# Optimization experiments

Measured on AMD Instinct MI355X. Metric: run time of the kernel, lower is better.

Reference implementation:

```python
import jax, jax.numpy as jnp
import numpy as np

B, S, K, N, GROUP = 4, 8, 4096, 11008, 128
NUM_GROUPS = K // GROUP  # 32


def setup_inputs() -> dict:
    key = jax.random.key(0)
    k1, k2, k3 = jax.random.split(key, 3)
    x = jax.random.normal(k1, (B, S, K), dtype=jnp.float16)
    # packed int4 weights: each byte holds two nibbles (low nibble = even k, high = odd k)
    weight_packed = jax.random.randint(k2, (N, K // 2), 0, 256, dtype=jnp.int32)
    # scales: abs(randn)*0.1 in fp16, as in the torch module
    scales = (jnp.abs(jax.random.normal(k3, (N, NUM_GROUPS), dtype=jnp.float16)) * jnp.float16(0.1))
    return {"x": x, "weight_packed": weight_packed, "scales": scales}


def _dequant(weight_packed, scales, Kd):
    # unpack: low nibble -> even index k, high nibble -> odd index k+1
    n = weight_packed.shape[0]
    low = weight_packed & 0xF
    high = (weight_packed >> 4) & 0xF
    w = jnp.stack([low, high], axis=-1).reshape(n, Kd)  # [N, K] int in [0,16)
    g = Kd // scales.shape[1]
    # group-wise dequant: scale * (w - 8), scale applied in fp32 (matches fp32-accum kernel)
    wq = (w.astype(jnp.float32) - 8.0).reshape(n, scales.shape[1], g)
    wdeq = wq * scales.astype(jnp.float32)[:, :, None]
    return wdeq.reshape(n, Kd)  # [N, K] fp32


def reference(x, weight_packed, scales):
    b, s, kd = x.shape
    wdeq = _dequant(weight_packed, scales, kd)           # [N, K]
    x2 = x.reshape(-1, kd).astype(jnp.float32)           # [M, K], fp32 accumulation
    out = jnp.einsum('mk,nk->mn', x2, wdeq)              # [M, N]
    return out.astype(jnp.float16).reshape(b, s, -1)
```

## Files before the change

### kernel.cpp

```cpp
#include <hip/hip_runtime.h>

#define M 32
#define N 11008
#define K 4096
#define NGROUPS 32
#define BN 16
#define KSPLIT 4
#define KRANGE (K / KSPLIT)
#define BK 128
#define NCHUNK (KRANGE / BK)
#define WQ 272
#define XQ 544
#define WCH (4 * WQ)
#define XCH (8 * XQ)

typedef _Float16 half8 __attribute__((ext_vector_type(8)));
typedef _Float16 half4 __attribute__((ext_vector_type(4)));
typedef float floatx4 __attribute__((ext_vector_type(4)));
typedef float float8 __attribute__((ext_vector_type(8)));

__device__ inline void gll16(const void* g, void* l) {
    __builtin_amdgcn_global_load_lds(
        (const __attribute__((address_space(1))) unsigned int*)g,
        (__attribute__((address_space(3))) unsigned int*)l, 16, 0, 0);
}

__device__ inline half8 unpack8(int4 wv) {
    uint4 uw; unsigned int b;
    b = (unsigned)wv.x; uw.x = ((b | (b << 12)) & 0x000F000Fu) | 0x64006400u;
    b = (unsigned)wv.y; uw.y = ((b | (b << 12)) & 0x000F000Fu) | 0x64006400u;
    b = (unsigned)wv.z; uw.z = ((b | (b << 12)) & 0x000F000Fu) | 0x64006400u;
    b = (unsigned)wv.w; uw.w = ((b | (b << 12)) & 0x000F000Fu) | 0x64006400u;
    const half8 c1032 = (half8)(_Float16)1032.0f;
    return __builtin_bit_cast(half8, uw) - c1032;
}

__global__ __launch_bounds__(512) void xcvt_kernel(
    const float* __restrict__ x, _Float16* __restrict__ xf)
{
    int i = (blockIdx.x * 512 + threadIdx.x) * 4;
    float4 v = *(const float4*)(x + i);
    half4 h;
    h[0] = (_Float16)v.x; h[1] = (_Float16)v.y;
    h[2] = (_Float16)v.z; h[3] = (_Float16)v.w;
    *(half4*)(xf + i) = h;
}

#define WAITV(n) asm volatile("s_waitcnt vmcnt(" #n ")" ::: "memory")
#define SB() __builtin_amdgcn_sched_barrier(0)

__global__ __launch_bounds__(256) void int4_gemm_kernel(
    const _Float16* __restrict__ xf,
    const int* __restrict__ wp,
    const float* __restrict__ scales,
    float* __restrict__ out)
{
    __shared__ int      wsh[2 * WCH];
    __shared__ _Float16 xs [2 * XCH];

    const int t    = threadIdx.x;
    const int lane = t & 63;
    const int w    = t >> 6;
    const int n0   = blockIdx.x * BN;
    const int ks   = blockIdx.y;
    const int row  = lane & 15;
    const int fq   = lane >> 4;
    const int kb   = ks * KRANGE;

    const int wcol = ((lane & 15) ^ fq) * 4;
    const int xcol = ((lane & 15) ^ fq) * 8;

    const int*      gwp = wp + (long)(n0 + w * 4 + fq) * (K / 2) + (kb >> 1) + wcol;
    const _Float16* gx0 = xf + (long)(w * 8 + fq) * K + kb + xcol;
    const _Float16* gx1 = gx0 + 4 * K;

    #define STAGE(c) {                                               \
        gll16(gwp + (c) * (BK / 2), &wsh[((c) & 1) * WCH + w * WQ]); \
        gll16(gx0 + (c) * BK, &xs[((c) & 1) * XCH + (2 * w) * XQ]);  \
        gll16(gx1 + (c) * BK, &xs[((c) & 1) * XCH + (2 * w + 1) * XQ]); \
        SB();                                                        \
    }

    const float8 sv = *(const float8*)(scales + (long)(n0 + row) * NGROUPS + ks * 8);

    const int riq  = row & 3;
    const int bcol = ((4 * w + fq) ^ riq) * 4;
    const int acol = ((4 * w + fq) ^ riq) * 8;
    const int widx = (row >> 2) * WQ + riq * 64 + bcol;
    const int xidx = (row >> 2) * XQ + riq * 128 + acol;

    floatx4 acc0 = {0,0,0,0}, acc1 = {0,0,0,0};

    STAGE(0)
    #pragma unroll
    for (int c = 0; c < NCHUNK; ++c) {
        if (c + 1 < NCHUNK) {
            STAGE(c + 1)
            WAITV(3);
        } else {
            WAITV(0);
        }
        __builtin_amdgcn_s_barrier();
        SB();

        const int bb = (c & 1);
        int4  wv = *(const int4*)&wsh[bb * WCH + widx];
        half8 a0 = *(const half8*)&xs[bb * XCH + xidx];
        half8 a1 = *(const half8*)&xs[bb * XCH + 4 * XQ + xidx];
        half8 bf = unpack8(wv);
        const floatx4 z = {0,0,0,0};
        floatx4 t0 = __builtin_amdgcn_mfma_f32_16x16x32_f16(a0, bf, z, 0, 0, 0);
        floatx4 t1 = __builtin_amdgcn_mfma_f32_16x16x32_f16(a1, bf, z, 0, 0, 0);
        #pragma unroll
        for (int r = 0; r < 4; ++r) {
            acc0[r] += sv[c] * t0[r];
            acc1[r] += sv[c] * t1[r];
        }

        SB();
        __builtin_amdgcn_s_barrier();
    }
    #undef STAGE

    __syncthreads();
    float* red = (float*)wsh;
    #pragma unroll
    for (int r = 0; r < 4; ++r) {
        red[w * 512 + (fq * 4 + r) * 16 + row]      = acc0[r];
        red[w * 512 + (fq * 4 + r + 16) * 16 + row] = acc1[r];
    }
    __syncthreads();
    #pragma unroll
    for (int i = 0; i < 2; ++i) {
        const int o = t + 256 * i;
        const float sum = red[o] + red[512 + o] + red[1024 + o] + red[1536 + o];
        const int m = o >> 4;
        const int n = o & 15;
        atomicAdd(&out[(long)m * N + n0 + n], sum);
    }
}

extern "C" void kernel_launch(void* const* d_in, const int* in_sizes, int n_in,
                              void* d_out, int out_size, void* d_ws, size_t ws_size,
                              hipStream_t stream) {
    const float* x      = (const float*)d_in[0];
    const int* wp       = (const int*)d_in[1];
    const float* scales = (const float*)d_in[2];
    float* out          = (float*)d_out;
    _Float16* xf16      = (_Float16*)d_ws;

    (void)hipMemsetAsync(out, 0, (size_t)M * N * sizeof(float), stream);
    xcvt_kernel<<<dim3((M * K) / (512 * 4)), 512, 0, stream>>>(x, xf16);
    int4_gemm_kernel<<<dim3(N / BN, KSPLIT), 256, 0, stream>>>(xf16, wp, scales, out);
}
```

Measured before the change: 146.0 us.

## Split K across eight blocks and one scale group per wave, dropping the LDS pipeline

Doubles the K split and gives each of the four waves its own 128-wide quantization group. Each wave issues all of its weight loads to LDS up front and loads x straight into registers, then accumulates four MFMAs per output tile with the scale applied once at the end. This removes the double-buffered chunk loop and its per-chunk barriers and exposes more blocks to hide memory latency. In exchange, the grid and the number of atomic adds into the output both double.

```diff
diff --git a/kernel.cpp b/kernel.cpp
--- a/kernel.cpp
+++ b/kernel.cpp
@@ -5,19 +5,13 @@
 #define K 4096
 #define NGROUPS 32
 #define BN 16
-#define KSPLIT 4
+#define KSPLIT 8
 #define KRANGE (K / KSPLIT)
-#define BK 128
-#define NCHUNK (KRANGE / BK)
-#define WQ 272
-#define XQ 544
-#define WCH (4 * WQ)
-#define XCH (8 * XQ)
+#define KWAVE (KRANGE / 4)
 
 typedef _Float16 half8 __attribute__((ext_vector_type(8)));
 typedef _Float16 half4 __attribute__((ext_vector_type(4)));
 typedef float floatx4 __attribute__((ext_vector_type(4)));
-typedef float float8 __attribute__((ext_vector_type(8)));
 
 __device__ inline void gll16(const void* g, void* l) {
     __builtin_amdgcn_global_load_lds(
@@ -55,79 +49,53 @@
     const float* __restrict__ scales,
     float* __restrict__ out)
 {
-    __shared__ int      wsh[2 * WCH];
-    __shared__ _Float16 xs [2 * XCH];
+    __shared__ int wsh[4096];
 
     const int t    = threadIdx.x;
     const int lane = t & 63;
     const int w    = t >> 6;
     const int n0   = blockIdx.x * BN;
     const int ks   = blockIdx.y;
-    const int row  = lane & 15;
-    const int fq   = lane >> 4;
-    const int kb   = ks * KRANGE;
+    const int col  = lane & 15;
+    const int quad = lane >> 4;
+    const int kw   = ks * KRANGE + w * KWAVE;
 
-    const int wcol = ((lane & 15) ^ fq) * 4;
-    const int xcol = ((lane & 15) ^ fq) * 8;
+    const float s = scales[(long)(n0 + col) * NGROUPS + ks * 4 + w];
+    SB();
 
-    const int*      gwp = wp + (long)(n0 + w * 4 + fq) * (K / 2) + (kb >> 1) + wcol;
-    const _Float16* gx0 = xf + (long)(w * 8 + fq) * K + kb + xcol;
-    const _Float16* gx1 = gx0 + 4 * K;
+    const int* gw = wp + (long)(n0 + col) * (K / 2) + (kw >> 1) + quad * 4;
+    #pragma unroll
+    for (int j = 0; j < 4; ++j)
+        gll16(gw + j * 16, &wsh[(w * 4 + j) * 256]);
+    SB();
 
-    #define STAGE(c) {                                               \
-        gll16(gwp + (c) * (BK / 2), &wsh[((c) & 1) * WCH + w * WQ]); \
-        gll16(gx0 + (c) * BK, &xs[((c) & 1) * XCH + (2 * w) * XQ]);  \
-        gll16(gx1 + (c) * BK, &xs[((c) & 1) * XCH + (2 * w + 1) * XQ]); \
-        SB();                                                        \
+    const _Float16* gx0 = xf + (long)col * K + kw + quad * 8;
+    const _Float16* gx1 = gx0 + 16 * K;
+    half8 xa[4], xb[4];
+    #pragma unroll
+    for (int j = 0; j < 4; ++j) {
+        xa[j] = *(const half8*)(gx0 + j * 32);
+        xb[j] = *(const half8*)(gx1 + j * 32);
     }
+    SB();
 
-    const float8 sv = *(const float8*)(scales + (long)(n0 + row) * NGROUPS + ks * 8);
-
-    const int riq  = row & 3;
-    const int bcol = ((4 * w + fq) ^ riq) * 4;
-    const int acol = ((4 * w + fq) ^ riq) * 8;
-    const int widx = (row >> 2) * WQ + riq * 64 + bcol;
-    const int xidx = (row >> 2) * XQ + riq * 128 + acol;
+    WAITV(8);
+    SB();
 
     floatx4 acc0 = {0,0,0,0}, acc1 = {0,0,0,0};
-
-    STAGE(0)
     #pragma unroll
-    for (int c = 0; c < NCHUNK; ++c) {
-        if (c + 1 < NCHUNK) {
-            STAGE(c + 1)
-            WAITV(3);
-        } else {
-            WAITV(0);
-        }
-        __builtin_amdgcn_s_barrier();
-        SB();
-
-        const int bb = (c & 1);
-        int4  wv = *(const int4*)&wsh[bb * WCH + widx];
-        half8 a0 = *(const half8*)&xs[bb * XCH + xidx];
-        half8 a1 = *(const half8*)&xs[bb * XCH + 4 * XQ + xidx];
-        half8 bf = unpack8(wv);
-        const floatx4 z = {0,0,0,0};
-        floatx4 t0 = __builtin_amdgcn_mfma_f32_16x16x32_f16(a0, bf, z, 0, 0, 0);
-        floatx4 t1 = __builtin_amdgcn_mfma_f32_16x16x32_f16(a1, bf, z, 0, 0, 0);
-        #pragma unroll
-        for (int r = 0; r < 4; ++r) {
-            acc0[r] += sv[c] * t0[r];
-            acc1[r] += sv[c] * t1[r];
-        }
-
-        SB();
-        __builtin_amdgcn_s_barrier();
+    for (int j = 0; j < 4; ++j) {
+        half8 bf = unpack8(*(const int4*)&wsh[(w * 4 + j) * 256 + lane * 4]);
+        acc0 = __builtin_amdgcn_mfma_f32_16x16x32_f16(xa[j], bf, acc0, 0, 0, 0);
+        acc1 = __builtin_amdgcn_mfma_f32_16x16x32_f16(xb[j], bf, acc1, 0, 0, 0);
     }
-    #undef STAGE
 
     __syncthreads();
     float* red = (float*)wsh;
     #pragma unroll
     for (int r = 0; r < 4; ++r) {
-        red[w * 512 + (fq * 4 + r) * 16 + row]      = acc0[r];
-        red[w * 512 + (fq * 4 + r + 16) * 16 + row] = acc1[r];
+        red[w * 512 + (quad * 4 + r) * 16 + col]      = s * acc0[r];
+        red[w * 512 + (quad * 4 + r + 16) * 16 + col] = s * acc1[r];
     }
     __syncthreads();
     #pragma unroll
```

Result: slower. 150.9 us (+3.4%).
